# Kernel tuning notes

Hardware: AMD Instinct MI355X
Metric: run time of the kernel (lower is better)

The kernel has to match this reference:

```python
import jax, jax.numpy as jnp
import numpy as np

N = 2048          # num nodes == in_channels (f1 = graphs[0].shape[0])
F_IN = 2048       # node feature dim
G1 = 10           # ChebConv out channels
E = 65536         # num edges (avg degree 32)
NUM_CLASSES = 10  # fc1 output


def setup_inputs() -> dict:
    key = jax.random.key(0)
    ks = jax.random.split(key, 6)
    x = jax.random.normal(ks[0], (N, F_IN), dtype=jnp.float32)
    edge_index = jax.random.randint(ks[1], (2, E), 0, N)
    # ChebConv weights: one [F_IN, G1] matrix per Chebyshev order (K=2), glorot-ish init
    s = float(1.0 / np.sqrt(F_IN))
    W0 = jax.random.uniform(ks[2], (F_IN, G1), jnp.float32, -s, s)
    W1 = jax.random.uniform(ks[3], (F_IN, G1), jnp.float32, -s, s)
    b = jnp.zeros((G1,), jnp.float32)
    sf = float(1.0 / np.sqrt(G1))
    Wf = jax.random.uniform(ks[4], (G1, NUM_CLASSES), jnp.float32, -sf, sf)
    bf = jax.random.uniform(ks[5], (NUM_CLASSES,), jnp.float32, -sf, sf)
    return {"x": x, "edge_index": edge_index, "W0": W0, "W1": W1, "b": b, "Wf": Wf, "bf": bf}


def _cheb_edge_weights(edge_index):
    # PyG ChebConv default: sym-normalized Laplacian scaled with lambda_max=2.0.
    # L_hat = 2*L/lambda_max - I = -D^{-1/2} A D^{-1/2}  (zero diagonal).
    row, col = edge_index[0], edge_index[1]
    deg = jax.ops.segment_sum(jnp.ones((E,), jnp.float32), row, num_segments=N)
    dis = jnp.where(deg > 0, jax.lax.rsqrt(jnp.maximum(deg, 1.0)), 0.0)
    return -dis[row] * dis[col]


def reference(x, edge_index, W0, W1, b, Wf, bf):
    row, col = edge_index[0], edge_index[1]
    w = _cheb_edge_weights(edge_index)
    # Tx_0 = x ; Tx_1 = L_hat @ x via gather (source=row) + scatter-add (target=col)
    Tx1 = jax.ops.segment_sum(w[:, None] * x[row], col, num_segments=N)  # [N, F_IN]
    h = x @ W0 + Tx1 @ W1 + b                                            # ChebConv, K=2
    h = jax.nn.relu(h)
    logits = h @ Wf + bf                                                 # fc1
    return jax.nn.log_softmax(logits, axis=1)
```

## Files before the change

### kernel.cpp

```cpp
#include <hip/hip_runtime.h>

#define N_NODES 2048
#define F_IN    2048
#define G1      10
#define NCLS    10
#define NEDGE   65536
#define JCHUNKS 64
#define JPER    32
#define HSLICES 128
#define ZSLICES 64

__device__ float g_p[JCHUNKS * 20 * N_NODES];
__device__ int   g_degp[HSLICES * N_NODES];
__device__ float g_dis[N_NODES];
__device__ float g_y[N_NODES * 20];
__device__ float g_zp[2 * ZSLICES * N_NODES * 5];

__global__ __launch_bounds__(256) void k_gemm(const float* __restrict__ x,
                                              const float* __restrict__ W0,
                                              const float* __restrict__ W1,
                                              const int* __restrict__ ei) {
    __shared__ float sx[256 * 33];
    int jc      = blockIdx.x;
    int rowbase = blockIdx.y * 256;
    int j0      = jc * JPER;

    #pragma unroll
    for (int rep = 0; rep < 8; ++rep) {
        int idx = rep * 256 + threadIdx.x;
        int r = idx >> 3, c4 = idx & 7;
        float4 v = *(const float4*)(x + (size_t)(rowbase + r) * F_IN + j0 + c4 * 4);
        float* d = sx + r * 33 + c4 * 4;
        d[0] = v.x; d[1] = v.y; d[2] = v.z; d[3] = v.w;
    }
    __syncthreads();

    float acc[20];
    #pragma unroll
    for (int k = 0; k < 20; ++k) acc[k] = 0.f;

    const float* xr = sx + threadIdx.x * 33;
    #pragma unroll
    for (int j = 0; j < JPER; ++j) {
        float xu = xr[j];
        const float* w0r = W0 + (size_t)(j0 + j) * G1;
        const float* w1r = W1 + (size_t)(j0 + j) * G1;
        #pragma unroll
        for (int k = 0; k < G1; ++k) {
            acc[k]      += xu * w0r[k];
            acc[10 + k] += xu * w1r[k];
        }
    }
    int row = rowbase + threadIdx.x;
    #pragma unroll
    for (int k = 0; k < 20; ++k)
        g_p[((size_t)jc * 20 + k) * N_NODES + row] = acc[k];

    if (blockIdx.y < 4 && jc < 32) {
        int slice = blockIdx.y * 32 + jc;
        __syncthreads();
        int* h = (int*)sx;
        for (int t = threadIdx.x; t < N_NODES; t += 256) h[t] = 0;
        __syncthreads();
        int base = slice * (NEDGE / HSLICES);
        #pragma unroll
        for (int u = 0; u < 2; ++u)
            atomicAdd(&h[ei[base + u * 256 + threadIdx.x]], 1);
        __syncthreads();
        for (int t = threadIdx.x; t < N_NODES; t += 256)
            g_degp[slice * N_NODES + t] = h[t];
    }
}

__global__ __launch_bounds__(256) void k_reduce() {
    int t   = blockIdx.x * 256 + threadIdx.x;
    int k   = t >> 11;
    int row = t & (N_NODES - 1);
    float s = 0.f;
    #pragma unroll 16
    for (int jc = 0; jc < JCHUNKS; ++jc)
        s += g_p[((size_t)jc * 20 + k) * N_NODES + row];
    g_y[row * 20 + k] = s;
    if (t < N_NODES) {
        int d = 0;
        #pragma unroll 16
        for (int sl = 0; sl < HSLICES; ++sl) d += g_degp[sl * N_NODES + t];
        g_dis[t] = (d > 0) ? rsqrtf((float)d) : 0.f;
    }
}

__global__ __launch_bounds__(256) void k_scatter(const int* __restrict__ ei) {
    __shared__ float zl[N_NODES * 5];
    int khalf  = blockIdx.x >> 6;
    int bslice = blockIdx.x & (ZSLICES - 1);
    float4* zl4 = (float4*)zl;
    #pragma unroll
    for (int t = threadIdx.x; t < N_NODES * 5 / 4; t += 256)
        zl4[t] = make_float4(0.f, 0.f, 0.f, 0.f);
    __syncthreads();
    int base = bslice * (NEDGE / ZSLICES);
    #pragma unroll
    for (int u = 0; u < NEDGE / ZSLICES / 256; ++u) {
        int e = base + u * 256 + threadIdx.x;
        int r = ei[e], c = ei[NEDGE + e];
        float w = -g_dis[r] * g_dis[c];
        const float* y1 = g_y + r * 20 + 10 + khalf * 5;
        float* zz = zl + c * 5;
        #pragma unroll
        for (int kk = 0; kk < 5; ++kk) atomicAdd(&zz[kk], w * y1[kk]);
    }
    __syncthreads();
    float4* dst = (float4*)(g_zp + ((size_t)khalf * ZSLICES + bslice) * (N_NODES * 5));
    #pragma unroll
    for (int t = threadIdx.x; t < N_NODES * 5 / 4; t += 256) dst[t] = zl4[t];
}

__global__ __launch_bounds__(256) void k_zf(const float* __restrict__ b,
                                            const float* __restrict__ Wf,
                                            const float* __restrict__ bfv,
                                            float* __restrict__ out) {
    __shared__ float zb[320];
    int nb = blockIdx.x * 32;
    for (int v = threadIdx.x; v < 320; v += 256) {
        int khalf = v / 160;
        int rem   = v - khalf * 160;
        int il    = rem / 5, kk = rem - il * 5;
        float s = 0.f;
        #pragma unroll 16
        for (int sl = 0; sl < ZSLICES; ++sl)
            s += g_zp[((size_t)khalf * ZSLICES + sl) * (N_NODES * 5) + (nb + il) * 5 + kk];
        zb[il * 10 + khalf * 5 + kk] = s;
    }
    __syncthreads();
    if (threadIdx.x < 32) {
        int i = nb + threadIdx.x;
        float h[G1];
        #pragma unroll
        for (int k = 0; k < G1; ++k)
            h[k] = fmaxf(g_y[i * 20 + k] + zb[threadIdx.x * 10 + k] + b[k], 0.f);
        float lo[NCLS];
        #pragma unroll
        for (int c = 0; c < NCLS; ++c) lo[c] = bfv[c];
        #pragma unroll
        for (int k = 0; k < G1; ++k) {
            float hk = h[k];
            #pragma unroll
            for (int c = 0; c < NCLS; ++c) lo[c] += hk * Wf[k * NCLS + c];
        }
        float m = lo[0];
        #pragma unroll
        for (int c = 1; c < NCLS; ++c) m = fmaxf(m, lo[c]);
        float s = 0.f;
        #pragma unroll
        for (int c = 0; c < NCLS; ++c) s += expf(lo[c] - m);
        float ls = logf(s);
        #pragma unroll
        for (int c = 0; c < NCLS; ++c) out[i * NCLS + c] = lo[c] - m - ls;
    }
}

extern "C" void kernel_launch(void* const* d_in, const int* in_sizes, int n_in,
                              void* d_out, int out_size, void* d_ws, size_t ws_size,
                              hipStream_t stream) {
    const float* x   = (const float*)d_in[0];
    const int*   ei  = (const int*)d_in[1];
    const float* W0  = (const float*)d_in[2];
    const float* W1  = (const float*)d_in[3];
    const float* b   = (const float*)d_in[4];
    const float* Wf  = (const float*)d_in[5];
    const float* bfv = (const float*)d_in[6];
    float* out = (float*)d_out;

    k_gemm<<<dim3(JCHUNKS, N_NODES / 256), 256, 0, stream>>>(x, W0, W1, ei);
    k_reduce<<<(N_NODES * 20) / 256, 256, 0, stream>>>();
    k_scatter<<<2 * ZSLICES, 256, 0, stream>>>(ei);
    k_zf<<<N_NODES / 32, 256, 0, stream>>>(b, Wf, bfv, out);
}
```

Measured before the change: 112.1 us.

## Fuse four kernels into one cooperative kernel with grid-wide syncs

Merges the GEMM, reduce, scatter and final softmax kernels into a single cooperative launch of 512 blocks, with grid.sync between stages. The aim is to remove three kernel launch gaps and their inter-kernel drain/ramp costs. In exchange, the whole grid must stay co-resident, later stages run on only a subset of blocks while the rest idle, and shared memory is sized for the largest stage (40KB), which may lower occupancy in the GEMM phase.

```diff
diff --git a/kernel.cpp b/kernel.cpp
--- a/kernel.cpp
+++ b/kernel.cpp
@@ -1,4 +1,7 @@
 #include <hip/hip_runtime.h>
+#include <hip/hip_cooperative_groups.h>
+
+namespace cg = cooperative_groups;
 
 #define N_NODES 2048
 #define F_IN    2048
@@ -9,6 +12,7 @@
 #define JPER    32
 #define HSLICES 128
 #define ZSLICES 64
+#define NBLK    512
 
 __device__ float g_p[JCHUNKS * 20 * N_NODES];
 __device__ int   g_degp[HSLICES * N_NODES];
@@ -16,146 +20,159 @@
 __device__ float g_y[N_NODES * 20];
 __device__ float g_zp[2 * ZSLICES * N_NODES * 5];
 
-__global__ __launch_bounds__(256) void k_gemm(const float* __restrict__ x,
-                                              const float* __restrict__ W0,
-                                              const float* __restrict__ W1,
-                                              const int* __restrict__ ei) {
-    __shared__ float sx[256 * 33];
-    int jc      = blockIdx.x;
-    int rowbase = blockIdx.y * 256;
-    int j0      = jc * JPER;
+__global__ __launch_bounds__(256) void k_all(const float* __restrict__ x,
+                                             const float* __restrict__ W0,
+                                             const float* __restrict__ W1,
+                                             const int* __restrict__ ei,
+                                             const float* __restrict__ b,
+                                             const float* __restrict__ Wf,
+                                             const float* __restrict__ bfv,
+                                             float* __restrict__ out) {
+    __shared__ float smem[N_NODES * 5];
+    cg::grid_group grid = cg::this_grid();
+    int bid = blockIdx.x;
+    int tid = threadIdx.x;
 
-    #pragma unroll
-    for (int rep = 0; rep < 8; ++rep) {
-        int idx = rep * 256 + threadIdx.x;
-        int r = idx >> 3, c4 = idx & 7;
-        float4 v = *(const float4*)(x + (size_t)(rowbase + r) * F_IN + j0 + c4 * 4);
-        float* d = sx + r * 33 + c4 * 4;
-        d[0] = v.x; d[1] = v.y; d[2] = v.z; d[3] = v.w;
-    }
-    __syncthreads();
+    {
+        int jc      = bid & 63;
+        int by      = bid >> 6;
+        int rowbase = by * 256;
+        int j0      = jc * JPER;
+        float* sx   = smem;
 
-    float acc[20];
-    #pragma unroll
-    for (int k = 0; k < 20; ++k) acc[k] = 0.f;
+        #pragma unroll
+        for (int rep = 0; rep < 8; ++rep) {
+            int idx = rep * 256 + tid;
+            int r = idx >> 3, c4 = idx & 7;
+            float4 v = *(const float4*)(x + (size_t)(rowbase + r) * F_IN + j0 + c4 * 4);
+            float* d = sx + r * 33 + c4 * 4;
+            d[0] = v.x; d[1] = v.y; d[2] = v.z; d[3] = v.w;
+        }
+        __syncthreads();
 
-    const float* xr = sx + threadIdx.x * 33;
-    #pragma unroll
-    for (int j = 0; j < JPER; ++j) {
-        float xu = xr[j];
-        const float* w0r = W0 + (size_t)(j0 + j) * G1;
-        const float* w1r = W1 + (size_t)(j0 + j) * G1;
+        float acc[20];
         #pragma unroll
-        for (int k = 0; k < G1; ++k) {
-            acc[k]      += xu * w0r[k];
-            acc[10 + k] += xu * w1r[k];
+        for (int k = 0; k < 20; ++k) acc[k] = 0.f;
+
+        const float* xr = sx + tid * 33;
+        #pragma unroll
+        for (int j = 0; j < JPER; ++j) {
+            float xu = xr[j];
+            const float* w0r = W0 + (size_t)(j0 + j) * G1;
+            const float* w1r = W1 + (size_t)(j0 + j) * G1;
+            #pragma unroll
+            for (int k = 0; k < G1; ++k) {
+                acc[k]      += xu * w0r[k];
+                acc[10 + k] += xu * w1r[k];
+            }
+        }
+        int row = rowbase + tid;
+        #pragma unroll
+        for (int k = 0; k < 20; ++k)
+            g_p[((size_t)jc * 20 + k) * N_NODES + row] = acc[k];
+
+        if (by < 4 && jc < 32) {
+            int slice = by * 32 + jc;
+            __syncthreads();
+            int* h = (int*)smem;
+            for (int t = tid; t < N_NODES; t += 256) h[t] = 0;
+            __syncthreads();
+            int base = slice * (NEDGE / HSLICES);
+            #pragma unroll
+            for (int u = 0; u < 2; ++u)
+                atomicAdd(&h[ei[base + u * 256 + tid]], 1);
+            __syncthreads();
+            for (int t = tid; t < N_NODES; t += 256)
+                g_degp[slice * N_NODES + t] = h[t];
         }
     }
-    int row = rowbase + threadIdx.x;
-    #pragma unroll
-    for (int k = 0; k < 20; ++k)
-        g_p[((size_t)jc * 20 + k) * N_NODES + row] = acc[k];
+    grid.sync();
 
-    if (blockIdx.y < 4 && jc < 32) {
-        int slice = blockIdx.y * 32 + jc;
+    {
+        int t = bid * 256 + tid;
+        if (t < N_NODES * 20) {
+            int k   = t >> 11;
+            int row = t & (N_NODES - 1);
+            float s = 0.f;
+            #pragma unroll 16
+            for (int jc = 0; jc < JCHUNKS; ++jc)
+                s += g_p[((size_t)jc * 20 + k) * N_NODES + row];
+            g_y[row * 20 + k] = s;
+        }
+        if (t < N_NODES) {
+            int d = 0;
+            #pragma unroll 16
+            for (int sl = 0; sl < HSLICES; ++sl) d += g_degp[sl * N_NODES + t];
+            g_dis[t] = (d > 0) ? rsqrtf((float)d) : 0.f;
+        }
+    }
+    grid.sync();
+
+    if (bid < 2 * ZSLICES) {
+        int khalf  = bid >> 6;
+        int bslice = bid & (ZSLICES - 1);
+        float4* zl4 = (float4*)smem;
+        #pragma unroll
+        for (int t = tid; t < N_NODES * 5 / 4; t += 256)
+            zl4[t] = make_float4(0.f, 0.f, 0.f, 0.f);
         __syncthreads();
-        int* h = (int*)sx;
-        for (int t = threadIdx.x; t < N_NODES; t += 256) h[t] = 0;
+        int base = bslice * (NEDGE / ZSLICES);
+        #pragma unroll
+        for (int u = 0; u < NEDGE / ZSLICES / 256; ++u) {
+            int e = base + u * 256 + tid;
+            int r = ei[e], c = ei[NEDGE + e];
+            float w = -g_dis[r] * g_dis[c];
+            const float* y1 = g_y + r * 20 + 10 + khalf * 5;
+            float* zz = smem + c * 5;
+            #pragma unroll
+            for (int kk = 0; kk < 5; ++kk) atomicAdd(&zz[kk], w * y1[kk]);
+        }
         __syncthreads();
-        int base = slice * (NEDGE / HSLICES);
+        float4* dst = (float4*)(g_zp + ((size_t)khalf * ZSLICES + bslice) * (N_NODES * 5));
         #pragma unroll
-        for (int u = 0; u < 2; ++u)
-            atomicAdd(&h[ei[base + u * 256 + threadIdx.x]], 1);
+        for (int t = tid; t < N_NODES * 5 / 4; t += 256) dst[t] = zl4[t];
+    }
+    grid.sync();
+
+    if (bid < 64) {
+        float* zb = smem;
+        int nb = bid * 32;
+        for (int v = tid; v < 320; v += 256) {
+            int khalf = v / 160;
+            int rem   = v - khalf * 160;
+            int il    = rem / 5, kk = rem - il * 5;
+            float s = 0.f;
+            #pragma unroll 16
+            for (int sl = 0; sl < ZSLICES; ++sl)
+                s += g_zp[((size_t)khalf * ZSLICES + sl) * (N_NODES * 5) + (nb + il) * 5 + kk];
+            zb[il * 10 + khalf * 5 + kk] = s;
+        }
         __syncthreads();
-        for (int t = threadIdx.x; t < N_NODES; t += 256)
-            g_degp[slice * N_NODES + t] = h[t];
-    }
-}
-
-__global__ __launch_bounds__(256) void k_reduce() {
-    int t   = blockIdx.x * 256 + threadIdx.x;
-    int k   = t >> 11;
-    int row = t & (N_NODES - 1);
-    float s = 0.f;
-    #pragma unroll 16
-    for (int jc = 0; jc < JCHUNKS; ++jc)
-        s += g_p[((size_t)jc * 20 + k) * N_NODES + row];
-    g_y[row * 20 + k] = s;
-    if (t < N_NODES) {
-        int d = 0;
-        #pragma unroll 16
-        for (int sl = 0; sl < HSLICES; ++sl) d += g_degp[sl * N_NODES + t];
-        g_dis[t] = (d > 0) ? rsqrtf((float)d) : 0.f;
-    }
-}
-
-__global__ __launch_bounds__(256) void k_scatter(const int* __restrict__ ei) {
-    __shared__ float zl[N_NODES * 5];
-    int khalf  = blockIdx.x >> 6;
-    int bslice = blockIdx.x & (ZSLICES - 1);
-    float4* zl4 = (float4*)zl;
-    #pragma unroll
-    for (int t = threadIdx.x; t < N_NODES * 5 / 4; t += 256)
-        zl4[t] = make_float4(0.f, 0.f, 0.f, 0.f);
-    __syncthreads();
-    int base = bslice * (NEDGE / ZSLICES);
-    #pragma unroll
-    for (int u = 0; u < NEDGE / ZSLICES / 256; ++u) {
-        int e = base + u * 256 + threadIdx.x;
-        int r = ei[e], c = ei[NEDGE + e];
-        float w = -g_dis[r] * g_dis[c];
-        const float* y1 = g_y + r * 20 + 10 + khalf * 5;
-        float* zz = zl + c * 5;
-        #pragma unroll
-        for (int kk = 0; kk < 5; ++kk) atomicAdd(&zz[kk], w * y1[kk]);
-    }
-    __syncthreads();
-    float4* dst = (float4*)(g_zp + ((size_t)khalf * ZSLICES + bslice) * (N_NODES * 5));
-    #pragma unroll
-    for (int t = threadIdx.x; t < N_NODES * 5 / 4; t += 256) dst[t] = zl4[t];
-}
-
-__global__ __launch_bounds__(256) void k_zf(const float* __restrict__ b,
-                                            const float* __restrict__ Wf,
-                                            const float* __restrict__ bfv,
-                                            float* __restrict__ out) {
-    __shared__ float zb[320];
-    int nb = blockIdx.x * 32;
-    for (int v = threadIdx.x; v < 320; v += 256) {
-        int khalf = v / 160;
-        int rem   = v - khalf * 160;
-        int il    = rem / 5, kk = rem - il * 5;
-        float s = 0.f;
-        #pragma unroll 16
-        for (int sl = 0; sl < ZSLICES; ++sl)
-            s += g_zp[((size_t)khalf * ZSLICES + sl) * (N_NODES * 5) + (nb + il) * 5 + kk];
-        zb[il * 10 + khalf * 5 + kk] = s;
-    }
-    __syncthreads();
-    if (threadIdx.x < 32) {
-        int i = nb + threadIdx.x;
-        float h[G1];
-        #pragma unroll
-        for (int k = 0; k < G1; ++k)
-            h[k] = fmaxf(g_y[i * 20 + k] + zb[threadIdx.x * 10 + k] + b[k], 0.f);
-        float lo[NCLS];
-        #pragma unroll
-        for (int c = 0; c < NCLS; ++c) lo[c] = bfv[c];
-        #pragma unroll
-        for (int k = 0; k < G1; ++k) {
-            float hk = h[k];
+        if (tid < 32) {
+            int i = nb + tid;
+            float h[G1];
             #pragma unroll
-            for (int c = 0; c < NCLS; ++c) lo[c] += hk * Wf[k * NCLS + c];
+            for (int k = 0; k < G1; ++k)
+                h[k] = fmaxf(g_y[i * 20 + k] + zb[tid * 10 + k] + b[k], 0.f);
+            float lo[NCLS];
+            #pragma unroll
+            for (int c = 0; c < NCLS; ++c) lo[c] = bfv[c];
+            #pragma unroll
+            for (int k = 0; k < G1; ++k) {
+                float hk = h[k];
+                #pragma unroll
+                for (int c = 0; c < NCLS; ++c) lo[c] += hk * Wf[k * NCLS + c];
+            }
+            float m = lo[0];
+            #pragma unroll
+            for (int c = 1; c < NCLS; ++c) m = fmaxf(m, lo[c]);
+            float s = 0.f;
+            #pragma unroll
+            for (int c = 0; c < NCLS; ++c) s += expf(lo[c] - m);
+            float ls = logf(s);
+            #pragma unroll
+            for (int c = 0; c < NCLS; ++c) out[i * NCLS + c] = lo[c] - m - ls;
         }
-        float m = lo[0];
-        #pragma unroll
-        for (int c = 1; c < NCLS; ++c) m = fmaxf(m, lo[c]);
-        float s = 0.f;
-        #pragma unroll
-        for (int c = 0; c < NCLS; ++c) s += expf(lo[c] - m);
-        float ls = logf(s);
-        #pragma unroll
-        for (int c = 0; c < NCLS; ++c) out[i * NCLS + c] = lo[c] - m - ls;
     }
 }
 
@@ -171,8 +188,10 @@
     const float* bfv = (const float*)d_in[6];
     float* out = (float*)d_out;
 
-    k_gemm<<<dim3(JCHUNKS, N_NODES / 256), 256, 0, stream>>>(x, W0, W1, ei);
-    k_reduce<<<(N_NODES * 20) / 256, 256, 0, stream>>>();
-    k_scatter<<<2 * ZSLICES, 256, 0, stream>>>(ei);
-    k_zf<<<N_NODES / 32, 256, 0, stream>>>(b, Wf, bfv, out);
+    void* args[] = {(void*)&x, (void*)&ei, (void*)&W0, (void*)&W1,
+                    (void*)&b, (void*)&Wf, (void*)&bfv, (void*)&out};
+    void* args2[] = {(void*)&x, (void*)&W0, (void*)&W1, (void*)&ei,
+                     (void*)&b, (void*)&Wf, (void*)&bfv, (void*)&out};
+    hipLaunchCooperativeKernel((void*)k_all, dim3(NBLK), dim3(256),
+                               args2, 0, stream);
 }
```

Result: slower. 304.8 us (+172.0%).
